# Optimization experiments

Hardware: AMD Instinct MI355X
Metric: run time of the kernel (lower is better)

The kernel has to match this reference:

```python
import jax, jax.numpy as jnp
import numpy as np

B, S, D = 8, 4096, 512
H, DH = 8, 64  # heads, dim_head; inner_dim = H*DH = 512
EPS = 1e-6


def setup_inputs() -> dict:
    key = jax.random.key(0)
    ks = jax.random.split(key, 9)
    scale = 1.0 / np.sqrt(D)
    inner = H * DH
    return {
        "x": jax.random.normal(ks[0], (B, S, D), dtype=jnp.float32),
        "Wq": jax.random.normal(ks[1], (D, inner), dtype=jnp.float32) * scale,
        "bq": jax.random.normal(ks[2], (inner,), dtype=jnp.float32) * 0.01,
        "Wk": jax.random.normal(ks[3], (D, inner), dtype=jnp.float32) * scale,
        "bk": jax.random.normal(ks[4], (inner,), dtype=jnp.float32) * 0.01,
        "Wv": jax.random.normal(ks[5], (D, inner), dtype=jnp.float32) * scale,
        "bv": jax.random.normal(ks[6], (inner,), dtype=jnp.float32) * 0.01,
        "Wo": jax.random.normal(ks[7], (inner, D), dtype=jnp.float32) * (1.0 / np.sqrt(inner)),
        "bo": jax.random.normal(ks[8], (D,), dtype=jnp.float32) * 0.01,
    }


def _phi(x):
    # elu(x) + 1, the fast-transformers default feature map
    return jax.nn.elu(x) + 1.0


def reference(x, Wq, bq, Wk, bk, Wv, bv, Wo, bo):
    b, s, _ = x.shape
    q = (x @ Wq + bq).reshape(b, s, H, DH)
    k = (x @ Wk + bk).reshape(b, s, H, DH)
    v = (x @ Wv + bv).reshape(b, s, H, DH)

    Qf = _phi(q)  # [b, s, h, d]
    Kf = _phi(k)  # [b, s, h, d]

    # KV = sum_s Kf_s (outer) v_s  -> [b, h, d, m]
    KV = jnp.einsum('bshd,bshm->bhdm', Kf, v)
    # normalizer: Z = 1 / (Qf . sum_s Kf + eps)  -> [b, s, h]
    Ksum = Kf.sum(axis=1)  # [b, h, d]
    Z = 1.0 / (jnp.einsum('bshd,bhd->bsh', Qf, Ksum) + EPS)
    out = jnp.einsum('bshd,bhdm,bsh->bshm', Qf, KV, Z)  # [b, s, h, m]

    out = out.reshape(b, s, H * DH)
    return out @ Wo + bo  # dropout is identity at inference
```

## Files before the change

kernel.cpp:

```cpp
#include <hip/hip_runtime.h>
#include <hip/hip_fp16.h>


constexpr int Ss = 4096;
constexpr int Dd = 512;
constexpr int Hh = 8;
constexpr int Mtot = 8 * 4096;
constexpr float EPSF = 1e-6f;

typedef short v8s __attribute__((ext_vector_type(8)));
typedef float v4f __attribute__((ext_vector_type(4)));

__device__ __forceinline__ short f2bf(float f) {
  unsigned u = __float_as_uint(f);
  u += 0x7fff + ((u >> 16) & 1);
  return (short)(u >> 16);
}
__device__ __forceinline__ float bf2f(short s) {
  return __uint_as_float(((unsigned)(unsigned short)s) << 16);
}
__device__ __forceinline__ void async_cp16(const void* g, void* l) {
  __builtin_amdgcn_global_load_lds((__attribute__((address_space(1))) void*)g,
                                   (__attribute__((address_space(3))) void*)l, 16, 0, 0);
}

__global__ __launch_bounds__(256) void prep_w(
    const float* __restrict__ W0, const float* __restrict__ W1,
    const float* __restrict__ W2, const float* __restrict__ W3,
    short* __restrict__ Th, short* __restrict__ Tl)
{
  const float* W = (blockIdx.z == 0) ? W0 : (blockIdx.z == 1) ? W1
                  : (blockIdx.z == 2) ? W2 : W3;
  short* th = Th + (size_t)blockIdx.z * 512 * 512;
  short* tl = Tl + (size_t)blockIdx.z * 512 * 512;
  __shared__ float tile[32][33];
  const int t = threadIdx.x;
  const int tx = t & 31, ty = t >> 5;
  const int k0 = blockIdx.x * 32, n0 = blockIdx.y * 32;
#pragma unroll
  for (int r = 0; r < 32; r += 8)
    tile[ty + r][tx] = W[(size_t)(k0 + ty + r) * 512 + n0 + tx];
  __syncthreads();
#pragma unroll
  for (int r = 0; r < 32; r += 8) {
    const float v = tile[tx][ty + r];
    const short h = f2bf(v);
    const short l = f2bf(v - bf2f(h));
    th[(size_t)(n0 + ty + r) * 512 + k0 + tx] = h;
    tl[(size_t)(n0 + ty + r) * 512 + k0 + tx] = l;
  }
}

__global__ __launch_bounds__(256) void split_x(
    const float* __restrict__ X, short* __restrict__ H, short* __restrict__ L, int n4)
{
  const int i = blockIdx.x * 256 + threadIdx.x;
  if (i >= n4) return;
  const float4 x = reinterpret_cast<const float4*>(X)[i];
  short4 h, l;
  h.x = f2bf(x.x); l.x = f2bf(x.x - bf2f(h.x));
  h.y = f2bf(x.y); l.y = f2bf(x.y - bf2f(h.y));
  h.z = f2bf(x.z); l.z = f2bf(x.z - bf2f(h.z));
  h.w = f2bf(x.w); l.w = f2bf(x.w - bf2f(h.w));
  reinterpret_cast<short4*>(H)[i] = h;
  reinterpret_cast<short4*>(L)[i] = l;
}

__global__ __launch_bounds__(256) void gemm_qkv(
    const short* __restrict__ Ah, const short* __restrict__ Al,
    const short* __restrict__ Wth, const short* __restrict__ Wtl,
    const float* __restrict__ bq, const float* __restrict__ bk,
    const float* __restrict__ bv,
    __half* __restrict__ Qf, __half* __restrict__ Kf, __half* __restrict__ Vv)
{
  constexpr int K = 512;
  __shared__ short As_h[128 * 32], As_l[128 * 32], Bs_h[128 * 32], Bs_l[128 * 32];

  const int mat = blockIdx.y >> 2;
  const int col0 = (blockIdx.y & 3) * 128;
  const int row0 = blockIdx.x * 128;
  const short* Bh = Wth + (size_t)mat * K * 512;
  const short* Bl = Wtl + (size_t)mat * K * 512;
  const float* bias = (mat == 0) ? bq : (mat == 1) ? bk : bv;
  __half* Co = (mat == 0) ? Qf : (mat == 1) ? Kf : Vv;
  const int act = (mat < 2);

  const int t = threadIdx.x;
  const int lane = t & 63;
  const int wv = t >> 6;
  const int wm = wv & 1, wn = wv >> 1;
  const int mr = lane & 15, kq = lane >> 4;

  v4f acc[4][4];
#pragma unroll
  for (int i = 0; i < 4; ++i)
#pragma unroll
    for (int j = 0; j < 4; ++j) acc[i][j] = (v4f){0.f, 0.f, 0.f, 0.f};

  const int srow = t >> 2;
  const int spq = t & 3;

  for (int k0 = 0; k0 < K; k0 += 32) {
#pragma unroll
    for (int c = 0; c < 2; ++c) {
      const int m = c * 64 + srow;
      const int q = spq ^ ((m >> 1) & 3);
      const size_t ga = (size_t)(row0 + m) * K + k0 + q * 8;
      const size_t gb = (size_t)(col0 + m) * K + k0 + q * 8;
      const int lo = c * 2048 + wv * 512;
      async_cp16(Ah + ga, As_h + lo);
      async_cp16(Al + ga, As_l + lo);
      async_cp16(Bh + gb, Bs_h + lo);
      async_cp16(Bl + gb, Bs_l + lo);
    }
    __syncthreads();

    v8s fah[4], fal[4], fbh[4], fbl[4];
#pragma unroll
    for (int i = 0; i < 4; ++i) {
      const int ma = wm * 64 + i * 16 + mr;
      const int pa = kq ^ ((ma >> 1) & 3);
      fah[i] = *reinterpret_cast<const v8s*>(&As_h[ma * 32 + pa * 8]);
      fal[i] = *reinterpret_cast<const v8s*>(&As_l[ma * 32 + pa * 8]);
      const int nb = wn * 64 + i * 16 + mr;
      const int pb = kq ^ ((nb >> 1) & 3);
      fbh[i] = *reinterpret_cast<const v8s*>(&Bs_h[nb * 32 + pb * 8]);
      fbl[i] = *reinterpret_cast<const v8s*>(&Bs_l[nb * 32 + pb * 8]);
    }
#pragma unroll
    for (int i = 0; i < 4; ++i)
#pragma unroll
      for (int j = 0; j < 4; ++j) {
        acc[i][j] = __builtin_amdgcn_mfma_f32_16x16x32_bf16(fah[i], fbh[j], acc[i][j], 0, 0, 0);
        acc[i][j] = __builtin_amdgcn_mfma_f32_16x16x32_bf16(fah[i], fbl[j], acc[i][j], 0, 0, 0);
        acc[i][j] = __builtin_amdgcn_mfma_f32_16x16x32_bf16(fal[i], fbh[j], acc[i][j], 0, 0, 0);
      }
    __syncthreads();
  }

#pragma unroll
  for (int j = 0; j < 4; ++j) {
    const int nc = col0 + wn * 64 + j * 16 + mr;
    const float bz = bias[nc];
#pragma unroll
    for (int i = 0; i < 4; ++i) {
      const int mbase = row0 + wm * 64 + i * 16 + kq * 4;
#pragma unroll
      for (int r = 0; r < 4; ++r) {
        float v = acc[i][j][r] + bz;
        if (act) v = (v > 0.f) ? (v + 1.f) : __expf(v);
        Co[(size_t)(mbase + r) * 512 + nc] = __float2half(v);
      }
    }
  }
}

__global__ __launch_bounds__(256) void gemm_split(
    const short* __restrict__ Ah, const short* __restrict__ Al,
    const short* __restrict__ Bh, const short* __restrict__ Bl,
    const float* __restrict__ bias, float* __restrict__ Cf)
{
  constexpr int K = 512;
  __shared__ short As_h[128 * 32], As_l[128 * 32], Bs_h[128 * 32], Bs_l[128 * 32];
  const int t = threadIdx.x;
  const int lane = t & 63;
  const int wv = t >> 6;
  const int wm = wv & 1, wn = wv >> 1;
  const int row0 = blockIdx.x * 128, col0 = blockIdx.y * 128;
  const int mr = lane & 15, kq = lane >> 4;

  v4f acc[4][4];
#pragma unroll
  for (int i = 0; i < 4; ++i)
#pragma unroll
    for (int j = 0; j < 4; ++j) acc[i][j] = (v4f){0.f, 0.f, 0.f, 0.f};

  const int srow = t >> 2;
  const int spq = t & 3;

  for (int k0 = 0; k0 < K; k0 += 32) {
#pragma unroll
    for (int c = 0; c < 2; ++c) {
      const int m = c * 64 + srow;
      const int q = spq ^ ((m >> 1) & 3);
      const size_t ga = (size_t)(row0 + m) * K + k0 + q * 8;
      const size_t gb = (size_t)(col0 + m) * K + k0 + q * 8;
      const int lo = c * 2048 + wv * 512;
      async_cp16(Ah + ga, As_h + lo);
      async_cp16(Al + ga, As_l + lo);
      async_cp16(Bh + gb, Bs_h + lo);
      async_cp16(Bl + gb, Bs_l + lo);
    }
    __syncthreads();

    v8s fah[4], fal[4], fbh[4], fbl[4];
#pragma unroll
    for (int i = 0; i < 4; ++i) {
      const int ma = wm * 64 + i * 16 + mr;
      const int pa = kq ^ ((ma >> 1) & 3);
      fah[i] = *reinterpret_cast<const v8s*>(&As_h[ma * 32 + pa * 8]);
      fal[i] = *reinterpret_cast<const v8s*>(&As_l[ma * 32 + pa * 8]);
      const int nb = wn * 64 + i * 16 + mr;
      const int pb = kq ^ ((nb >> 1) & 3);
      fbh[i] = *reinterpret_cast<const v8s*>(&Bs_h[nb * 32 + pb * 8]);
      fbl[i] = *reinterpret_cast<const v8s*>(&Bs_l[nb * 32 + pb * 8]);
    }
#pragma unroll
    for (int i = 0; i < 4; ++i)
#pragma unroll
      for (int j = 0; j < 4; ++j) {
        acc[i][j] = __builtin_amdgcn_mfma_f32_16x16x32_bf16(fah[i], fbh[j], acc[i][j], 0, 0, 0);
        acc[i][j] = __builtin_amdgcn_mfma_f32_16x16x32_bf16(fah[i], fbl[j], acc[i][j], 0, 0, 0);
        acc[i][j] = __builtin_amdgcn_mfma_f32_16x16x32_bf16(fal[i], fbh[j], acc[i][j], 0, 0, 0);
      }
    __syncthreads();
  }

#pragma unroll
  for (int j = 0; j < 4; ++j) {
    const int nc = col0 + wn * 64 + j * 16 + mr;
    const float bz = bias[nc];
#pragma unroll
    for (int i = 0; i < 4; ++i) {
      const int mbase = row0 + wm * 64 + i * 16 + kq * 4;
#pragma unroll
      for (int r = 0; r < 4; ++r) Cf[(size_t)(mbase + r) * 512 + nc] = acc[i][j][r] + bz;
    }
  }
}

__global__ __launch_bounds__(256) void kv_stage1(
    const __half* __restrict__ Kf, const __half* __restrict__ V,
    float* __restrict__ KVp, float* __restrict__ Ksp)
{
  const int sc = blockIdx.x, bh = blockIdx.y;
  const int b = bh >> 3, h = bh & 7;
  __shared__ float Ks[64][68];
  __shared__ float Vs[64][68];
  const int tid = threadIdx.x;
  const int dx = (tid >> 4) * 4;
  const int mx = (tid & 15) * 4;
  float acc[4][4];
#pragma unroll
  for (int i = 0; i < 4; ++i)
#pragma unroll
    for (int j = 0; j < 4; ++j) acc[i][j] = 0.f;
  float ksum_acc = 0.f;
  const size_t base = (size_t)b * Ss * Dd + (size_t)h * 64;

  for (int s0 = sc * 256; s0 < sc * 256 + 256; s0 += 64) {
#pragma unroll
    for (int l = 0; l < 2; ++l) {
      const int idx = tid + l * 256;
      const int rr = idx >> 3, cq = idx & 7;
      const size_t g = base + (size_t)(s0 + rr) * Dd + cq * 8;
      const __half2* k2 = reinterpret_cast<const __half2*>(Kf + g);
      const __half2* v2 = reinterpret_cast<const __half2*>(V + g);
#pragma unroll
      for (int u = 0; u < 4; ++u) {
        const float2 kf = __half22float2(k2[u]);
        const float2 vf = __half22float2(v2[u]);
        Ks[rr][cq * 8 + u * 2] = kf.x; Ks[rr][cq * 8 + u * 2 + 1] = kf.y;
        Vs[rr][cq * 8 + u * 2] = vf.x; Vs[rr][cq * 8 + u * 2 + 1] = vf.y;
      }
    }
    __syncthreads();
#pragma unroll 4
    for (int s = 0; s < 64; ++s) {
      const float4 kd = *reinterpret_cast<const float4*>(&Ks[s][dx]);
      const float4 vm = *reinterpret_cast<const float4*>(&Vs[s][mx]);
      const float ka[4] = {kd.x, kd.y, kd.z, kd.w};
      const float va[4] = {vm.x, vm.y, vm.z, vm.w};
#pragma unroll
      for (int i = 0; i < 4; ++i)
#pragma unroll
        for (int j = 0; j < 4; ++j) acc[i][j] = fmaf(ka[i], va[j], acc[i][j]);
    }
    if (tid < 64) {
#pragma unroll 8
      for (int s = 0; s < 64; ++s) ksum_acc += Ks[s][tid];
    }
    __syncthreads();
  }

  const size_t pb = (size_t)(sc * 64 + bh);
#pragma unroll
  for (int i = 0; i < 4; ++i) {
    const float4 ov = {acc[i][0], acc[i][1], acc[i][2], acc[i][3]};
    *reinterpret_cast<float4*>(&KVp[(pb * 64 + dx + i) * 64 + mx]) = ov;
  }
  if (tid < 64) Ksp[pb * 64 + tid] = ksum_acc;
}

__global__ __launch_bounds__(256) void kv_stage2(
    const float* __restrict__ KVp, const float* __restrict__ Ksp,
    float* __restrict__ KV, float* __restrict__ Ksum)
{
  const int bh = blockIdx.x, t = threadIdx.x;
  for (int e = t; e < 4096; e += 256) {
    float s = 0.f;
#pragma unroll
    for (int sc = 0; sc < 16; ++sc) s += KVp[((size_t)(sc * 64 + bh) << 12) + e];
    KV[(size_t)bh * 4096 + e] = s;
  }
  if (t < 64) {
    float s = 0.f;
#pragma unroll
    for (int sc = 0; sc < 16; ++sc) s += Ksp[(size_t)(sc * 64 + bh) * 64 + t];
    Ksum[bh * 64 + t] = s;
  }
}

__global__ __launch_bounds__(256) void attn_combine(
    const __half* __restrict__ Qf, const float* __restrict__ KV,
    const float* __restrict__ Ksum, short* __restrict__ Oh, short* __restrict__ Ol)
{
  const int h = blockIdx.y;
  const int r0 = blockIdx.x * 64;
  const int b = r0 >> 12;
  const int bh = b * Hh + h;
  __shared__ float Qs[64][68];
  __shared__ float KVs[64][68];
  __shared__ float Ksums[64];
  __shared__ float Zs[64];
  const int tid = threadIdx.x;

#pragma unroll
  for (int l = 0; l < 2; ++l) {
    const int idx = tid + l * 256;
    const int rr = idx >> 3, cq = idx & 7;
    const __half2* q2 = reinterpret_cast<const __half2*>(
        Qf + (size_t)(r0 + rr) * Dd + h * 64 + cq * 8);
#pragma unroll
    for (int u = 0; u < 4; ++u) {
      const float2 qf = __half22float2(q2[u]);
      Qs[rr][cq * 8 + u * 2] = qf.x; Qs[rr][cq * 8 + u * 2 + 1] = qf.y;
    }
  }
#pragma unroll
  for (int l = 0; l < 4; ++l) {
    const int idx = tid + l * 256;
    const int rr = idx >> 4, cq = idx & 15;
    *reinterpret_cast<float4*>(&KVs[rr][cq * 4]) = *reinterpret_cast<const float4*>(
        &KV[(size_t)bh * 4096 + rr * 64 + cq * 4]);
  }
  if (tid < 64) Ksums[tid] = Ksum[bh * 64 + tid];
  __syncthreads();

  if (tid < 64) {
    float z = 0.f;
#pragma unroll 8
    for (int d = 0; d < 64; ++d) z = fmaf(Qs[tid][d], Ksums[d], z);
    Zs[tid] = 1.f / (z + EPSF);
  }
  __syncthreads();

  const int rx = (tid >> 4) * 4, mx = (tid & 15) * 4;
  float acc[4][4];
#pragma unroll
  for (int i = 0; i < 4; ++i)
#pragma unroll
    for (int j = 0; j < 4; ++j) acc[i][j] = 0.f;

#pragma unroll 4
  for (int d = 0; d < 64; ++d) {
    const float4 vm = *reinterpret_cast<const float4*>(&KVs[d][mx]);
    const float va[4] = {vm.x, vm.y, vm.z, vm.w};
#pragma unroll
    for (int i = 0; i < 4; ++i) {
      const float q = Qs[rx + i][d];
#pragma unroll
      for (int j = 0; j < 4; ++j) acc[i][j] = fmaf(q, va[j], acc[i][j]);
    }
  }

#pragma unroll
  for (int i = 0; i < 4; ++i) {
    const float z = Zs[rx + i];
    short4 hv, lv;
    float o;
    o = acc[i][0] * z; hv.x = f2bf(o); lv.x = f2bf(o - bf2f(hv.x));
    o = acc[i][1] * z; hv.y = f2bf(o); lv.y = f2bf(o - bf2f(hv.y));
    o = acc[i][2] * z; hv.z = f2bf(o); lv.z = f2bf(o - bf2f(hv.z));
    o = acc[i][3] * z; hv.w = f2bf(o); lv.w = f2bf(o - bf2f(hv.w));
    const size_t off = (size_t)(r0 + rx + i) * Dd + h * 64 + mx;
    *reinterpret_cast<short4*>(&Oh[off]) = hv;
    *reinterpret_cast<short4*>(&Ol[off]) = lv;
  }
}

extern "C" void kernel_launch(void* const* d_in, const int* in_sizes, int n_in,
                              void* d_out, int out_size, void* d_ws, size_t ws_size,
                              hipStream_t stream) {
  const float* x  = (const float*)d_in[0];
  const float* Wq = (const float*)d_in[1];
  const float* bq = (const float*)d_in[2];
  const float* Wk = (const float*)d_in[3];
  const float* bk = (const float*)d_in[4];
  const float* Wv = (const float*)d_in[5];
  const float* bv = (const float*)d_in[6];
  const float* Wo = (const float*)d_in[7];
  const float* bo = (const float*)d_in[8];
  float* out = (float*)d_out;

  char* ws = (char*)d_ws;
  const size_t MB = (size_t)1 << 20;
  short*  x_hi  = (short*)(ws);
  short*  x_lo  = (short*)(ws + 32 * MB);
  short*  Wt_hi = (short*)(ws + 64 * MB);
  short*  Wt_lo = (short*)(ws + 66 * MB);
  __half* Qf    = (__half*)(ws + 68 * MB);
  __half* Kf    = (__half*)(ws + 100 * MB);
  __half* Vv    = (__half*)(ws + 132 * MB);
  float*  KVp   = (float*)(ws + 164 * MB);
  float*  Ksp   = (float*)(ws + 181 * MB);
  float*  KV    = (float*)(ws + 182 * MB);
  float*  Ksum  = (float*)(ws + 183 * MB);
  short*  attn_hi = x_hi;
  short*  attn_lo = x_lo;
  const size_t WSTEP = (size_t)512 * 512;

  prep_w<<<dim3(16, 16, 4), 256, 0, stream>>>(Wq, Wk, Wv, Wo, Wt_hi, Wt_lo);
  split_x<<<Mtot * Dd / 4 / 256, 256, 0, stream>>>(x, x_hi, x_lo, Mtot * Dd / 4);

  gemm_qkv<<<dim3(Mtot / 128, 12), 256, 0, stream>>>(
      x_hi, x_lo, Wt_hi, Wt_lo, bq, bk, bv, Qf, Kf, Vv);

  kv_stage1<<<dim3(16, 64), 256, 0, stream>>>(Kf, Vv, KVp, Ksp);
  kv_stage2<<<64, 256, 0, stream>>>(KVp, Ksp, KV, Ksum);
  attn_combine<<<dim3(Mtot / 64, Hh), 256, 0, stream>>>(Qf, KV, Ksum, attn_hi, attn_lo);

  gemm_split<<<dim3(Mtot / 128, 4), 256, 0, stream>>>(
      attn_hi, attn_lo, Wt_hi + 3 * WSTEP, Wt_lo + 3 * WSTEP, bo, out);
}
```

Baseline: 428.7 us.

## Double-buffer GEMMs with 256x256 tiles and three sequential split-precision passes

Both split-bf16 GEMMs now use 256x256 tiles with 512 threads and a double-buffered LDS pipeline. Global-to-LDS async copies for the next K tile overlap the MFMAs on the current one, using explicit vmcnt waits and raw barriers. The hi*hi, hi*lo and lo*hi products become three sequential 16-step passes over K instead of loading four operand tiles per step, and MFMA sections are raised with s_setprio. The aim is better operand reuse, hidden load latency and fewer LDS bytes per step, at the cost of more accumulator registers, fewer blocks in the grid, and reliance on hand-placed wait counts for correctness.

```diff
diff --git a/kernel.cpp b/kernel.cpp
--- a/kernel.cpp
+++ b/kernel.cpp
@@ -66,76 +66,99 @@
   reinterpret_cast<short4*>(L)[i] = l;
 }
 
-__global__ __launch_bounds__(256) void gemm_qkv(
+__device__ __forceinline__ void stage_tile(
+    const short* __restrict__ pA, const short* __restrict__ pB,
+    short* as, short* bs, int k0, int t)
+{
+#pragma unroll
+  for (int c = 0; c < 2; ++c) {
+    const int idx = t + c * 512;
+    const int row = idx >> 2;
+    const int q = (idx & 3) ^ ((row >> 1) & 3);
+    const size_t g = (size_t)row * 512 + k0 + q * 8;
+    async_cp16(pA + g, as + idx * 8);
+    async_cp16(pB + g, bs + idx * 8);
+  }
+}
+
+__global__ __launch_bounds__(512, 2) void gemm_qkv(
     const short* __restrict__ Ah, const short* __restrict__ Al,
     const short* __restrict__ Wth, const short* __restrict__ Wtl,
     const float* __restrict__ bq, const float* __restrict__ bk,
     const float* __restrict__ bv,
     __half* __restrict__ Qf, __half* __restrict__ Kf, __half* __restrict__ Vv)
 {
-  constexpr int K = 512;
-  __shared__ short As_h[128 * 32], As_l[128 * 32], Bs_h[128 * 32], Bs_l[128 * 32];
-
-  const int mat = blockIdx.y >> 2;
-  const int col0 = (blockIdx.y & 3) * 128;
-  const int row0 = blockIdx.x * 128;
-  const short* Bh = Wth + (size_t)mat * K * 512;
-  const short* Bl = Wtl + (size_t)mat * K * 512;
+  __shared__ short As[2][256 * 32];
+  __shared__ short Bs[2][256 * 32];
+
+  const int mat = blockIdx.y >> 1;
+  const int col0 = (blockIdx.y & 1) * 256;
+  const int row0 = blockIdx.x * 256;
   const float* bias = (mat == 0) ? bq : (mat == 1) ? bk : bv;
   __half* Co = (mat == 0) ? Qf : (mat == 1) ? Kf : Vv;
   const int act = (mat < 2);
 
+  const short* Ahb = Ah + (size_t)row0 * 512;
+  const short* Alb = Al + (size_t)row0 * 512;
+  const short* Bhb = Wth + (size_t)mat * 512 * 512 + (size_t)col0 * 512;
+  const short* Blb = Wtl + (size_t)mat * 512 * 512 + (size_t)col0 * 512;
+
   const int t = threadIdx.x;
   const int lane = t & 63;
   const int wv = t >> 6;
-  const int wm = wv & 1, wn = wv >> 1;
+  const int wm = wv >> 2, wn = wv & 3;
   const int mr = lane & 15, kq = lane >> 4;
 
-  v4f acc[4][4];
-#pragma unroll
-  for (int i = 0; i < 4; ++i)
+  int a_off[8], b_off[4];
+#pragma unroll
+  for (int i = 0; i < 8; ++i) {
+    const int ma = wm * 128 + i * 16 + mr;
+    a_off[i] = ma * 32 + (kq ^ ((ma >> 1) & 3)) * 8;
+  }
+#pragma unroll
+  for (int j = 0; j < 4; ++j) {
+    const int nb = wn * 64 + j * 16 + mr;
+    b_off[j] = nb * 32 + (kq ^ ((nb >> 1) & 3)) * 8;
+  }
+
+  v4f acc[8][4];
+#pragma unroll
+  for (int i = 0; i < 8; ++i)
 #pragma unroll
     for (int j = 0; j < 4; ++j) acc[i][j] = (v4f){0.f, 0.f, 0.f, 0.f};
 
-  const int srow = t >> 2;
-  const int spq = t & 3;
-
-  for (int k0 = 0; k0 < K; k0 += 32) {
-#pragma unroll
-    for (int c = 0; c < 2; ++c) {
-      const int m = c * 64 + srow;
-      const int q = spq ^ ((m >> 1) & 3);
-      const size_t ga = (size_t)(row0 + m) * K + k0 + q * 8;
-      const size_t gb = (size_t)(col0 + m) * K + k0 + q * 8;
-      const int lo = c * 2048 + wv * 512;
-      async_cp16(Ah + ga, As_h + lo);
-      async_cp16(Al + ga, As_l + lo);
-      async_cp16(Bh + gb, Bs_h + lo);
-      async_cp16(Bl + gb, Bs_l + lo);
-    }
-    __syncthreads();
-
-    v8s fah[4], fal[4], fbh[4], fbl[4];
-#pragma unroll
-    for (int i = 0; i < 4; ++i) {
-      const int ma = wm * 64 + i * 16 + mr;
-      const int pa = kq ^ ((ma >> 1) & 3);
-      fah[i] = *reinterpret_cast<const v8s*>(&As_h[ma * 32 + pa * 8]);
-      fal[i] = *reinterpret_cast<const v8s*>(&As_l[ma * 32 + pa * 8]);
-      const int nb = wn * 64 + i * 16 + mr;
-      const int pb = kq ^ ((nb >> 1) & 3);
-      fbh[i] = *reinterpret_cast<const v8s*>(&Bs_h[nb * 32 + pb * 8]);
-      fbl[i] = *reinterpret_cast<const v8s*>(&Bs_l[nb * 32 + pb * 8]);
-    }
-#pragma unroll
-    for (int i = 0; i < 4; ++i)
-#pragma unroll
-      for (int j = 0; j < 4; ++j) {
-        acc[i][j] = __builtin_amdgcn_mfma_f32_16x16x32_bf16(fah[i], fbh[j], acc[i][j], 0, 0, 0);
-        acc[i][j] = __builtin_amdgcn_mfma_f32_16x16x32_bf16(fah[i], fbl[j], acc[i][j], 0, 0, 0);
-        acc[i][j] = __builtin_amdgcn_mfma_f32_16x16x32_bf16(fal[i], fbh[j], acc[i][j], 0, 0, 0);
-      }
-    __syncthreads();
+  stage_tile(Ahb, Bhb, As[0], Bs[0], 0, t);
+
+  for (int kt = 0; kt < 48; ++kt) {
+    const int cur = kt & 1;
+    if (kt + 1 < 48) {
+      const int nx = kt + 1;
+      const int pass = nx >> 4;
+      const short* pA = (pass == 2) ? Alb : Ahb;
+      const short* pB = (pass == 1) ? Blb : Bhb;
+      stage_tile(pA, pB, As[cur ^ 1], Bs[cur ^ 1], (nx & 15) * 32, t);
+      asm volatile("s_waitcnt vmcnt(4)" ::: "memory");
+    } else {
+      asm volatile("s_waitcnt vmcnt(0)" ::: "memory");
+    }
+    __builtin_amdgcn_s_barrier();
+    asm volatile("" ::: "memory");
+
+    v8s fb[4];
+#pragma unroll
+    for (int j = 0; j < 4; ++j)
+      fb[j] = *reinterpret_cast<const v8s*>(&Bs[cur][b_off[j]]);
+    __builtin_amdgcn_s_setprio(1);
+#pragma unroll
+    for (int i = 0; i < 8; ++i) {
+      const v8s fa = *reinterpret_cast<const v8s*>(&As[cur][a_off[i]]);
+#pragma unroll
+      for (int j = 0; j < 4; ++j)
+        acc[i][j] = __builtin_amdgcn_mfma_f32_16x16x32_bf16(fa, fb[j], acc[i][j], 0, 0, 0);
+    }
+    __builtin_amdgcn_s_setprio(0);
+    asm volatile("" ::: "memory");
+    __builtin_amdgcn_s_barrier();
   }
 
 #pragma unroll
@@ -143,8 +166,8 @@
     const int nc = col0 + wn * 64 + j * 16 + mr;
     const float bz = bias[nc];
 #pragma unroll
-    for (int i = 0; i < 4; ++i) {
-      const int mbase = row0 + wm * 64 + i * 16 + kq * 4;
+    for (int i = 0; i < 8; ++i) {
+      const int mbase = row0 + wm * 128 + i * 16 + kq * 4;
 #pragma unroll
       for (int r = 0; r < 4; ++r) {
         float v = acc[i][j][r] + bz;
@@ -155,65 +178,78 @@
   }
 }
 
-__global__ __launch_bounds__(256) void gemm_split(
+__global__ __launch_bounds__(512, 2) void gemm_split(
     const short* __restrict__ Ah, const short* __restrict__ Al,
     const short* __restrict__ Bh, const short* __restrict__ Bl,
     const float* __restrict__ bias, float* __restrict__ Cf)
 {
-  constexpr int K = 512;
-  __shared__ short As_h[128 * 32], As_l[128 * 32], Bs_h[128 * 32], Bs_l[128 * 32];
+  __shared__ short As[2][256 * 32];
+  __shared__ short Bs[2][256 * 32];
+
+  const int col0 = blockIdx.y * 256;
+  const int row0 = blockIdx.x * 256;
+
+  const short* Ahb = Ah + (size_t)row0 * 512;
+  const short* Alb = Al + (size_t)row0 * 512;
+  const short* Bhb = Bh + (size_t)col0 * 512;
+  const short* Blb = Bl + (size_t)col0 * 512;
+
   const int t = threadIdx.x;
   const int lane = t & 63;
   const int wv = t >> 6;
-  const int wm = wv & 1, wn = wv >> 1;
-  const int row0 = blockIdx.x * 128, col0 = blockIdx.y * 128;
+  const int wm = wv >> 2, wn = wv & 3;
   const int mr = lane & 15, kq = lane >> 4;
 
-  v4f acc[4][4];
-#pragma unroll
-  for (int i = 0; i < 4; ++i)
+  int a_off[8], b_off[4];
+#pragma unroll
+  for (int i = 0; i < 8; ++i) {
+    const int ma = wm * 128 + i * 16 + mr;
+    a_off[i] = ma * 32 + (kq ^ ((ma >> 1) & 3)) * 8;
+  }
+#pragma unroll
+  for (int j = 0; j < 4; ++j) {
+    const int nb = wn * 64 + j * 16 + mr;
+    b_off[j] = nb * 32 + (kq ^ ((nb >> 1) & 3)) * 8;
+  }
+
+  v4f acc[8][4];
+#pragma unroll
+  for (int i = 0; i < 8; ++i)
 #pragma unroll
     for (int j = 0; j < 4; ++j) acc[i][j] = (v4f){0.f, 0.f, 0.f, 0.f};
 
-  const int srow = t >> 2;
-  const int spq = t & 3;
-
-  for (int k0 = 0; k0 < K; k0 += 32) {
-#pragma unroll
-    for (int c = 0; c < 2; ++c) {
-      const int m = c * 64 + srow;
-      const int q = spq ^ ((m >> 1) & 3);
-      const size_t ga = (size_t)(row0 + m) * K + k0 + q * 8;
-      const size_t gb = (size_t)(col0 + m) * K + k0 + q * 8;
-      const int lo = c * 2048 + wv * 512;
-      async_cp16(Ah + ga, As_h + lo);
-      async_cp16(Al + ga, As_l + lo);
-      async_cp16(Bh + gb, Bs_h + lo);
-      async_cp16(Bl + gb, Bs_l + lo);
-    }
-    __syncthreads();
-
-    v8s fah[4], fal[4], fbh[4], fbl[4];
-#pragma unroll
-    for (int i = 0; i < 4; ++i) {
-      const int ma = wm * 64 + i * 16 + mr;
-      const int pa = kq ^ ((ma >> 1) & 3);
-      fah[i] = *reinterpret_cast<const v8s*>(&As_h[ma * 32 + pa * 8]);
-      fal[i] = *reinterpret_cast<const v8s*>(&As_l[ma * 32 + pa * 8]);
-      const int nb = wn * 64 + i * 16 + mr;
-      const int pb = kq ^ ((nb >> 1) & 3);
-      fbh[i] = *reinterpret_cast<const v8s*>(&Bs_h[nb * 32 + pb * 8]);
-      fbl[i] = *reinterpret_cast<const v8s*>(&Bs_l[nb * 32 + pb * 8]);
-    }
-#pragma unroll
-    for (int i = 0; i < 4; ++i)
-#pragma unroll
-      for (int j = 0; j < 4; ++j) {
-        acc[i][j] = __builtin_amdgcn_mfma_f32_16x16x32_bf16(fah[i], fbh[j], acc[i][j], 0, 0, 0);
-        acc[i][j] = __builtin_amdgcn_mfma_f32_16x16x32_bf16(fah[i], fbl[j], acc[i][j], 0, 0, 0);
-        acc[i][j] = __builtin_amdgcn_mfma_f32_16x16x32_bf16(fal[i], fbh[j], acc[i][j], 0, 0, 0);
-      }
-    __syncthreads();
+  stage_tile(Ahb, Bhb, As[0], Bs[0], 0, t);
+
+  for (int kt = 0; kt < 48; ++kt) {
+    const int cur = kt & 1;
+    if (kt + 1 < 48) {
+      const int nx = kt + 1;
+      const int pass = nx >> 4;
+      const short* pA = (pass == 2) ? Alb : Ahb;
+      const short* pB = (pass == 1) ? Blb : Bhb;
+      stage_tile(pA, pB, As[cur ^ 1], Bs[cur ^ 1], (nx & 15) * 32, t);
+      asm volatile("s_waitcnt vmcnt(4)" ::: "memory");
+    } else {
+      asm volatile("s_waitcnt vmcnt(0)" ::: "memory");
+    }
+    __builtin_amdgcn_s_barrier();
+    asm volatile("" ::: "memory");
+
+    v8s fb[4];
+#pragma unroll
+    for (int j = 0; j < 4; ++j)
+      fb[j] = *reinterpret_cast<const v8s*>(&Bs[cur][b_off[j]]);
+    __builtin_amdgcn_s_setprio(1);
+#pragma unroll
+    for (int i = 0; i < 8; ++i) {
+      const v8s fa = *reinterpret_cast<const v8s*>(&As[cur][a_off[i]]);
+#pragma unroll
+      for (int j = 0; j < 4; ++j)
+        acc[i][j] = __builtin_amdgcn_mfma_f32_16x16x32_bf16(fa, fb[j], acc[i][j], 0, 0, 0);
+    }
+    __builtin_amdgcn_s_setprio(0);
+    asm volatile("" ::: "memory");
+    __builtin_amdgcn_s_barrier();
   }
 
 #pragma unroll
@@ -221,8 +257,8 @@
     const int nc = col0 + wn * 64 + j * 16 + mr;
     const float bz = bias[nc];
 #pragma unroll
-    for (int i = 0; i < 4; ++i) {
-      const int mbase = row0 + wm * 64 + i * 16 + kq * 4;
+    for (int i = 0; i < 8; ++i) {
+      const int mbase = row0 + wm * 128 + i * 16 + kq * 4;
 #pragma unroll
       for (int r = 0; r < 4; ++r) Cf[(size_t)(mbase + r) * 512 + nc] = acc[i][j][r] + bz;
     }
@@ -423,13 +459,13 @@
   prep_w<<<dim3(16, 16, 4), 256, 0, stream>>>(Wq, Wk, Wv, Wo, Wt_hi, Wt_lo);
   split_x<<<Mtot * Dd / 4 / 256, 256, 0, stream>>>(x, x_hi, x_lo, Mtot * Dd / 4);
 
-  gemm_qkv<<<dim3(Mtot / 128, 12), 256, 0, stream>>>(
+  gemm_qkv<<<dim3(Mtot / 256, 6), 512, 0, stream>>>(
       x_hi, x_lo, Wt_hi, Wt_lo, bq, bk, bv, Qf, Kf, Vv);
 
   kv_stage1<<<dim3(16, 64), 256, 0, stream>>>(Kf, Vv, KVp, Ksp);
   kv_stage2<<<64, 256, 0, stream>>>(KVp, Ksp, KV, Ksum);
   attn_combine<<<dim3(Mtot / 64, Hh), 256, 0, stream>>>(Qf, KV, Ksum, attn_hi, attn_lo);
 
-  gemm_split<<<dim3(Mtot / 128, 4), 256, 0, stream>>>(
+  gemm_split<<<dim3(Mtot / 256, 2), 512, 0, stream>>>(
       attn_hi, attn_lo, Wt_hi + 3 * WSTEP, Wt_lo + 3 * WSTEP, bo, out);
 }
```

New measurement: 497.9 us. 16.1% more time.
